# Performance work log

Hardware: AMD Instinct MI355X
Metric: run time of the kernel (lower is better)

The kernel has to match this reference:

```python
import jax, jax.numpy as jnp
import numpy as np

B, N, F, H, K, HID, TAB = 4, 256, 1024, 16, 128, 4096, 32
D = F // H
PI = 3.14159  # matches literal in source


def setup_inputs() -> dict:
    key = jax.random.key(0)
    ks = jax.random.split(key, 20)
    r = lambda i, shape: jax.random.normal(ks[i], shape, jnp.float32) * 0.02
    return dict(
        nfeat=jax.random.normal(ks[0], (B, N, F), jnp.float32),
        sp_dist=jax.random.randint(ks[1], (B, N, N), 0, TAB, dtype=jnp.int32),
        rd_dist=jax.random.uniform(ks[2], (B, N, N), jnp.float32),
        dist_table=r(3, (TAB, K)),
        g_means=jax.random.uniform(ks[4], (K,), jnp.float32, 0.0, 3.0),
        g_stds=jax.random.uniform(ks[5], (K,), jnp.float32, 0.0, 3.0),
        g_mul=jnp.ones((1,), jnp.float32),
        g_bias=jnp.zeros((1,), jnp.float32),
        mlp_w1=r(6, (2 * K, H)), mlp_b1=jnp.zeros((H,), jnp.float32),
        mlp_w2=r(7, (H, H)), mlp_b2=jnp.zeros((H,), jnp.float32),
        wq=r(8, (F, F)), bq=jnp.zeros((F,), jnp.float32),
        wk=r(9, (F, F)), bk=jnp.zeros((F,), jnp.float32),
        wv=r(10, (F, F)), bv=jnp.zeros((F,), jnp.float32),
        wo=r(11, (F, F)), bo=jnp.zeros((F,), jnp.float32),
        ffn_w1=r(12, (F, HID)), ffn_b1=jnp.zeros((HID,), jnp.float32),
        ffn_w2=r(13, (HID, F)), ffn_b2=jnp.zeros((F,), jnp.float32),
        ln1_g=jnp.ones((F,), jnp.float32), ln1_b=jnp.zeros((F,), jnp.float32),
        ln2_g=jnp.ones((F,), jnp.float32), ln2_b=jnp.zeros((F,), jnp.float32),
    )


def _layer_norm(x, g, b):
    m = x.mean(-1, keepdims=True)
    v = ((x - m) ** 2).mean(-1, keepdims=True)
    return (x - m) / jnp.sqrt(v + 1e-5) * g + b


def reference(nfeat, sp_dist, rd_dist, dist_table, g_means, g_stds, g_mul, g_bias,
              mlp_w1, mlp_b1, mlp_w2, mlp_b2, wq, bq, wk, bk, wv, bv, wo, bo,
              ffn_w1, ffn_b1, ffn_w2, ffn_b2, ln1_g, ln1_b, ln2_g, ln2_b):
    # --- FusedDistEncoder: shortest-path embedding + Gaussian resistance-distance encoding ---
    sp_emb = dist_table[sp_dist]                      # [B,N,N,K]
    x = g_mul * rd_dist[..., None] + g_bias           # [B,N,N,1] -> broadcast over K
    std = jnp.abs(g_stds) + 0.01                      # [K]
    rd_emb = jnp.exp(-0.5 * ((x - g_means) / std) ** 2) / (((2 * PI) ** 0.5) * std)
    h = jnp.concatenate([sp_emb, rd_emb], axis=-1)    # [B,N,N,2K]
    h = jax.nn.gelu(h @ mlp_w1 + mlp_b1, approximate=False)
    attn_bias = h @ mlp_w2 + mlp_b2                   # [B,N,N,H]

    # --- BiasedMultiheadAttention (note: source divides q by scaling=d^-0.5, i.e. *sqrt(d)) ---
    q = (nfeat @ wq + bq).reshape(B, N, H, D) * (D ** 0.5)
    k = (nfeat @ wk + bk).reshape(B, N, H, D)
    v = (nfeat @ wv + bv).reshape(B, N, H, D)
    scores = jnp.einsum('bihd,bjhd->bijh', q, k) + attn_bias   # [B,N,N,H]
    w = jax.nn.softmax(scores, axis=2)                          # softmax over key dim j
    attn = jnp.einsum('bijh,bjhd->bihd', w, v).reshape(B, N, F) @ wo + bo

    # --- GraphormerLayer residuals (post-norm, dropout=0 / eval) ---
    x1 = _layer_norm(nfeat + attn, ln1_g, ln1_b)
    ffn = jax.nn.relu(x1 @ ffn_w1 + ffn_b1) @ ffn_w2 + ffn_b2
    return _layer_norm(x1 + ffn, ln2_g, ln2_b)
```

## Files before the change

kernel.cpp:

```cpp
#include <hip/hip_runtime.h>
#include <hip/hip_bf16.h>
#include <math.h>

typedef __hip_bfloat16 bf16;
typedef float f32x4 __attribute__((ext_vector_type(4)));
typedef short bf16x8 __attribute__((ext_vector_type(8)));

#define AS1 __attribute__((address_space(1)))
#define AS3 __attribute__((address_space(3)))

__global__ __launch_bounds__(256) void setup_kernel(
    const float* __restrict__ nfeat, bf16* __restrict__ nfeatb,
    const float* __restrict__ bq, const float* __restrict__ bk,
    const float* __restrict__ bv, float* __restrict__ bqkv,
    const float* __restrict__ table, const float* __restrict__ w1,
    float* __restrict__ tw)
{
    int bid = blockIdx.x, t = threadIdx.x;
    if (bid < 1024) {
        int i = (bid * 256 + t) * 4;
        float4 v = *reinterpret_cast<const float4*>(nfeat + i);
        nfeatb[i + 0] = (bf16)v.x; nfeatb[i + 1] = (bf16)v.y;
        nfeatb[i + 2] = (bf16)v.z; nfeatb[i + 3] = (bf16)v.w;
    } else if (bid < 1036) {
        int i = (bid - 1024) * 256 + t;
        bqkv[i] = i < 1024 ? bq[i] : (i < 2048 ? bk[i - 1024] : bv[i - 2048]);
    } else {
        #pragma unroll
        for (int e = t; e < 512; e += 256) {
            int r = e >> 4, o = e & 15;
            float a = 0.f;
            for (int k = 0; k < 128; ++k) a += table[r * 128 + k] * w1[k * 16 + o];
            tw[e] = a;
        }
    }
}

__global__ __launch_bounds__(256) void wtx_kernel(
    const float* __restrict__ wq, const float* __restrict__ wk,
    const float* __restrict__ wv, const float* __restrict__ wo,
    const float* __restrict__ fw1, const float* __restrict__ fw2,
    bf16* __restrict__ qkvT, bf16* __restrict__ woT,
    bf16* __restrict__ fw1T, bf16* __restrict__ fw2T)
{
    __shared__ float tile[64][68];
    int bid = blockIdx.x, t = threadIdx.x;
    const float* W; bf16* WT; int Kd, Nd, local;
    if (bid < 768)       { int ws = bid >> 8; local = bid & 255;
                           W = ws == 0 ? wq : ws == 1 ? wk : wv;
                           WT = qkvT + ws * 1048576; Kd = 1024; Nd = 1024; }
    else if (bid < 1024) { local = bid - 768;  W = wo;  WT = woT;  Kd = 1024; Nd = 1024; }
    else if (bid < 2048) { local = bid - 1024; W = fw1; WT = fw1T; Kd = 1024; Nd = 4096; }
    else                 { local = bid - 2048; W = fw2; WT = fw2T; Kd = 4096; Nd = 1024; }
    int ntn = Nd >> 6;
    int k0 = (local / ntn) * 64, n0 = (local % ntn) * 64;

    {
        int k = t >> 2, nb = (t & 3) * 16;
        const float* src = W + (size_t)(k0 + k) * Nd + n0 + nb;
        #pragma unroll
        for (int c = 0; c < 4; c++) {
            float4 v = *reinterpret_cast<const float4*>(src + c * 4);
            *reinterpret_cast<float4*>(&tile[k][nb + c * 4]) = v;
        }
    }
    __syncthreads();

    {
        int w = t >> 6, l = t & 63;
        int n = w * 16 + (l >> 2), kb = (l & 3) * 16;
        bf16x8 o0, o1;
        #pragma unroll
        for (int j = 0; j < 8; j++) {
            union { bf16 b; short s; } u;
            u.b = (bf16)tile[kb + j][n];
            o0[j] = u.s;
        }
        #pragma unroll
        for (int j = 0; j < 8; j++) {
            union { bf16 b; short s; } u;
            u.b = (bf16)tile[kb + 8 + j][n];
            o1[j] = u.s;
        }
        bf16* dst = WT + (size_t)(n0 + n) * Kd + k0 + kb;
        *reinterpret_cast<bf16x8*>(dst) = o0;
        *reinterpret_cast<bf16x8*>(dst + 8) = o1;
    }
}

__global__ __launch_bounds__(256) void enc_kernel(
    const int* __restrict__ sp, const float* __restrict__ rd,
    const float* __restrict__ tw,
    const float* __restrict__ means, const float* __restrict__ stds,
    const float* __restrict__ gmul, const float* __restrict__ gbias,
    const float* __restrict__ w1, const float* __restrict__ b1,
    const float* __restrict__ w2, const float* __restrict__ b2,
    bf16* __restrict__ biasT)
{
    __shared__ float w1s[128][16];
    __shared__ float w2s[16][16];
    __shared__ float b1s[16], b2s[16];
    __shared__ float meanS[128], istdS[128], coefS[128];
    int t = threadIdx.x;
    for (int i = t; i < 2048; i += 256) w1s[i >> 4][i & 15] = w1[2048 + i];
    w2s[t >> 4][t & 15] = w2[t];
    if (t < 16) { b1s[t] = b1[t]; b2s[t] = b2[t]; }
    if (t < 128) {
        float s = fabsf(stds[t]) + 0.01f;
        meanS[t] = means[t];
        istdS[t] = 1.f / s;
        coefS[t] = 1.f / (sqrtf(2.f * 3.14159f) * s);
    }
    __syncthreads();

    int p = blockIdx.x * 256 + t;
    int idx = sp[p];
    float xv = gmul[0] * rd[p] + gbias[0];

    float acc[16];
    #pragma unroll
    for (int o = 0; o < 16; o++) acc[o] = b1s[o] + tw[idx * 16 + o];

    for (int k = 0; k < 128; k++) {
        float d = (xv - meanS[k]) * istdS[k];
        float g = coefS[k] * __expf(-0.5f * d * d);
        #pragma unroll
        for (int o = 0; o < 16; o++) acc[o] += g * w1s[k][o];
    }
    float h[16];
    #pragma unroll
    for (int o = 0; o < 16; o++) {
        float a = acc[o];
        h[o] = 0.5f * a * (1.f + erff(a * 0.70710678118f));
    }
    float outv[16];
    #pragma unroll
    for (int o = 0; o < 16; o++) outv[o] = b2s[o];
    #pragma unroll
    for (int q = 0; q < 16; q++) {
        float hq = h[q];
        #pragma unroll
        for (int o = 0; o < 16; o++) outv[o] += hq * w2s[q][o];
    }
    int b = blockIdx.x >> 8, i = blockIdx.x & 255;
    #pragma unroll
    for (int hh = 0; hh < 16; hh++)
        biasT[(((b * 16 + hh) * 256 + i) << 8) + t] = (bf16)outv[hh];
}

__global__ __launch_bounds__(256, 2) void gemm_bf16(
    const bf16* __restrict__ A, const bf16* __restrict__ BT,
    const float* __restrict__ bias, void* __restrict__ C,
    int M, int Nd, int Kd, int epi)
{
    __shared__ __align__(16) char smem[32768];
    int t = threadIdx.x;
    int w = t >> 6, l = t & 63;
    int wr = w >> 1, wc = w & 1;
    int lr = l & 15, lc = l >> 4;
    int row0 = blockIdx.y * 128, col0 = blockIdx.x * 128;
    int nz = gridDim.z;
    int klen = Kd / nz, kbeg = blockIdx.z * klen;

    f32x4 acc[4][4];
    #pragma unroll
    for (int i = 0; i < 4; i++)
        #pragma unroll
        for (int j = 0; j < 4; j++) acc[i][j] = (f32x4){0.f, 0.f, 0.f, 0.f};

    int sr = t & 127, sc = t >> 7;
    const bf16* Asrc = A + (size_t)(row0 + sr) * Kd + kbeg + sc * 8;
    const bf16* Bsrc = BT + (size_t)(col0 + sr) * Kd + kbeg + sc * 8;
    int wbase = (t & 192) * 16;

    int aoff = lc * 2048 + (wr * 64 + lr) * 16;
    int boff = 8192 + lc * 2048 + (wc * 64 + lr) * 16;

    #pragma unroll
    for (int p = 0; p < 2; p++) {
        __builtin_amdgcn_global_load_lds((const AS1 void*)(Asrc + p * 16),
            (AS3 void*)(smem + p * 4096 + wbase), 16, 0, 0);
        __builtin_amdgcn_global_load_lds((const AS1 void*)(Bsrc + p * 16),
            (AS3 void*)(smem + 8192 + p * 4096 + wbase), 16, 0, 0);
    }
    __syncthreads();

    int nsteps = klen >> 5;
    for (int s = 0; s < nsteps; ++s) {
        int cur = s & 1;
        if (s + 1 < nsteps) {
            const bf16* An = Asrc + (s + 1) * 32;
            const bf16* Bn = Bsrc + (s + 1) * 32;
            char* dst = smem + (cur ^ 1) * 16384;
            #pragma unroll
            for (int p = 0; p < 2; p++) {
                __builtin_amdgcn_global_load_lds((const AS1 void*)(An + p * 16),
                    (AS3 void*)(dst + p * 4096 + wbase), 16, 0, 0);
                __builtin_amdgcn_global_load_lds((const AS1 void*)(Bn + p * 16),
                    (AS3 void*)(dst + 8192 + p * 4096 + wbase), 16, 0, 0);
            }
        }
        const char* base = smem + cur * 16384;
        bf16x8 af[4], bfr[4];
        #pragma unroll
        for (int i = 0; i < 4; i++) af[i] = *(const bf16x8*)(base + aoff + i * 256);
        #pragma unroll
        for (int j = 0; j < 4; j++) bfr[j] = *(const bf16x8*)(base + boff + j * 256);
        #pragma unroll
        for (int i = 0; i < 4; i++)
            #pragma unroll
            for (int j = 0; j < 4; j++)
                acc[i][j] = __builtin_amdgcn_mfma_f32_16x16x32_bf16(
                    af[i], bfr[j], acc[i][j], 0, 0, 0);
        __syncthreads();
    }

    if (nz > 1) {
        float* P = (float*)C + (size_t)blockIdx.z * M * Nd;
        #pragma unroll
        for (int i = 0; i < 4; i++) {
            int rb = row0 + wr * 64 + i * 16 + lc * 4;
            #pragma unroll
            for (int j = 0; j < 4; j++) {
                int cc = col0 + wc * 64 + j * 16 + lr;
                f32x4 v = acc[i][j];
                #pragma unroll
                for (int q = 0; q < 4; q++) P[(size_t)(rb + q) * Nd + cc] = v[q];
            }
        }
        return;
    }

    #pragma unroll
    for (int i = 0; i < 4; i++) {
        int rb = row0 + wr * 64 + i * 16 + lc * 4;
        #pragma unroll
        for (int j = 0; j < 4; j++) {
            int cc = col0 + wc * 64 + j * 16 + lr;
            float bsv = bias[cc];
            f32x4 v = acc[i][j];
            #pragma unroll
            for (int q = 0; q < 4; q++) {
                int r = rb + q;
                float x = v[q] + bsv;
                if (epi == 2) ((bf16*)C)[(size_t)r * Nd + cc] = (bf16)fmaxf(x, 0.f);
                else          ((float*)C)[(size_t)r * Nd + cc] = x;
            }
        }
    }
}

__global__ __launch_bounds__(256) void qkv_combine_kernel(
    const float* __restrict__ part, const float* __restrict__ bqkv,
    bf16* __restrict__ qkvb)
{
    int e0 = (blockIdx.x * 256 + threadIdx.x) * 4;
    int r = e0 / 3072, cc0 = e0 - r * 3072;
    float4 p0 = *(const float4*)(part + e0);
    float4 p1 = *(const float4*)(part + 3145728 + e0);
    float4 bs = *(const float4*)(bqkv + cc0);
    float x[4] = {p0.x + p1.x + bs.x, p0.y + p1.y + bs.y,
                  p0.z + p1.z + bs.z, p0.w + p1.w + bs.w};
    int bb = r >> 8, ii = r & 255;
    int sel = cc0 >> 10, ccc0 = cc0 & 1023;
    int hh = ccc0 >> 6, dd0 = ccc0 & 63;
    #pragma unroll
    for (int u = 0; u < 4; u++) {
        float v = x[u];
        int dd = dd0 + u;
        if (sel == 0)
            qkvb[(((bb * 16 + hh) * 256 + ii) << 6) + dd] = (bf16)(v * 8.0f);
        else if (sel == 1)
            qkvb[1048576 + (((bb * 16 + hh) * 256 + ii) << 6) + dd] = (bf16)v;
        else
            qkvb[2097152 + ((((bb * 16 + hh) << 6) + dd) << 8) + ii] = (bf16)v;
    }
}

__global__ __launch_bounds__(256) void flash_kernel(
    const bf16* __restrict__ Qb, const bf16* __restrict__ Kb,
    const bf16* __restrict__ VT, const bf16* __restrict__ biasT,
    bf16* __restrict__ out)
{
    __shared__ __align__(16) char pls[32768];
    int t = threadIdx.x;
    int w = t >> 6, l = t & 63;
    int lr = l & 15, hi = l >> 4;
    int bh = blockIdx.x >> 2, iq = blockIdx.x & 3;
    int b = bh >> 4, h = bh & 15;
    int i0 = iq * 64 + w * 16;

    const bf16* Qp = Qb + (bh * 256 + i0 + lr) * 64 + hi * 8;
    bf16x8 qf0 = *(const bf16x8*)(Qp);
    bf16x8 qf1 = *(const bf16x8*)(Qp + 32);

    f32x4 acc[16];
    #pragma unroll
    for (int f = 0; f < 16; f++) acc[f] = (f32x4){0.f, 0.f, 0.f, 0.f};

    const bf16* Kp = Kb + (bh * 256 + lr) * 64 + hi * 8;
    #pragma unroll
    for (int f = 0; f < 16; f++) {
        bf16x8 kf0 = *(const bf16x8*)(Kp + f * 1024);
        bf16x8 kf1 = *(const bf16x8*)(Kp + f * 1024 + 32);
        acc[f] = __builtin_amdgcn_mfma_f32_16x16x32_bf16(qf0, kf0, acc[f], 0, 0, 0);
        acc[f] = __builtin_amdgcn_mfma_f32_16x16x32_bf16(qf1, kf1, acc[f], 0, 0, 0);
    }

    const bf16* bp = biasT + (bh * 256 + i0 + hi * 4) * 256 + lr;
    #pragma unroll
    for (int f = 0; f < 16; f++)
        #pragma unroll
        for (int q = 0; q < 4; q++)
            acc[f][q] += __bfloat162float(bp[q * 256 + f * 16]);

    float inv[4];
    #pragma unroll
    for (int q = 0; q < 4; q++) {
        float m = acc[0][q];
        #pragma unroll
        for (int f = 1; f < 16; f++) m = fmaxf(m, acc[f][q]);
        #pragma unroll
        for (int msk = 1; msk < 16; msk <<= 1) m = fmaxf(m, __shfl_xor(m, msk));
        float s = 0.f;
        #pragma unroll
        for (int f = 0; f < 16; f++) {
            float e = __expf(acc[f][q] - m);
            acc[f][q] = e;
            s += e;
        }
        #pragma unroll
        for (int msk = 1; msk < 16; msk <<= 1) s += __shfl_xor(s, msk);
        inv[q] = 1.f / s;
    }

    char* Pw = pls + w * 8192;
    #pragma unroll
    for (int f = 0; f < 16; f++) {
        int j = f * 16 + lr;
        int c = j >> 3, jo = j & 7;
        #pragma unroll
        for (int q = 0; q < 4; q++)
            *(bf16*)(Pw + c * 256 + (hi * 4 + q) * 16 + jo * 2) = (bf16)(acc[f][q] * inv[q]);
    }
    __syncthreads();

    const char* Pr = pls + w * 8192 + hi * 256 + lr * 16;
    const bf16* Vp = VT + (bh * 64 + lr) * 256 + hi * 8;
    #pragma unroll
    for (int n = 0; n < 4; n++) {
        f32x4 o = (f32x4){0.f, 0.f, 0.f, 0.f};
        #pragma unroll
        for (int ks = 0; ks < 8; ks++) {
            bf16x8 pa = *(const bf16x8*)(Pr + ks * 1024);
            bf16x8 vb = *(const bf16x8*)(Vp + n * 4096 + ks * 32);
            o = __builtin_amdgcn_mfma_f32_16x16x32_bf16(pa, vb, o, 0, 0, 0);
        }
        #pragma unroll
        for (int q = 0; q < 4; q++)
            out[(b * 256 + i0 + hi * 4 + q) * 1024 + h * 64 + n * 16 + lr] = (bf16)o[q];
    }
}

__global__ __launch_bounds__(256) void ln_fused_kernel(
    const float* __restrict__ part, int S,
    const float* __restrict__ bias, const float* __restrict__ add,
    const float* __restrict__ g, const float* __restrict__ bta,
    float* __restrict__ out, bf16* __restrict__ ob)
{
    int row = blockIdx.x;
    int t = threadIdx.x;
    float v[4];
    float sum = 0.f;
    #pragma unroll
    for (int i = 0; i < 4; i++) {
        int c = t + i * 256;
        float x = add[row * 1024 + c] + bias[c];
        for (int s = 0; s < S; s++) x += part[s * 1048576 + row * 1024 + c];
        v[i] = x;
        sum += x;
    }
    __shared__ float red[8];
    #pragma unroll
    for (int off = 32; off; off >>= 1) sum += __shfl_xor(sum, off);
    if ((t & 63) == 0) red[t >> 6] = sum;
    __syncthreads();
    float mean = (red[0] + red[1] + red[2] + red[3]) * (1.f / 1024.f);
    float vs = 0.f;
    #pragma unroll
    for (int i = 0; i < 4; i++) { float d = v[i] - mean; vs += d * d; }
    #pragma unroll
    for (int off = 32; off; off >>= 1) vs += __shfl_xor(vs, off);
    if ((t & 63) == 0) red[4 + (t >> 6)] = vs;
    __syncthreads();
    float var = (red[4] + red[5] + red[6] + red[7]) * (1.f / 1024.f);
    float invs = rsqrtf(var + 1e-5f);
    #pragma unroll
    for (int i = 0; i < 4; i++) {
        int c = t + i * 256;
        float o = (v[i] - mean) * invs * g[c] + bta[c];
        out[row * 1024 + c] = o;
        if (ob) ob[row * 1024 + c] = (bf16)o;
    }
}

extern "C" void kernel_launch(void* const* d_in, const int* in_sizes, int n_in,
                              void* d_out, int out_size, void* d_ws, size_t ws_size,
                              hipStream_t stream)
{
    const float* nfeat  = (const float*)d_in[0];
    const int*   sp     = (const int*)  d_in[1];
    const float* rd     = (const float*)d_in[2];
    const float* table  = (const float*)d_in[3];
    const float* gmeans = (const float*)d_in[4];
    const float* gstds  = (const float*)d_in[5];
    const float* gmul   = (const float*)d_in[6];
    const float* gbias  = (const float*)d_in[7];
    const float* w1     = (const float*)d_in[8];
    const float* b1     = (const float*)d_in[9];
    const float* w2     = (const float*)d_in[10];
    const float* b2     = (const float*)d_in[11];
    const float* wq     = (const float*)d_in[12];
    const float* bq     = (const float*)d_in[13];
    const float* wk     = (const float*)d_in[14];
    const float* bk     = (const float*)d_in[15];
    const float* wv     = (const float*)d_in[16];
    const float* bv     = (const float*)d_in[17];
    const float* wo     = (const float*)d_in[18];
    const float* bo     = (const float*)d_in[19];
    const float* fw1    = (const float*)d_in[20];
    const float* fb1    = (const float*)d_in[21];
    const float* fw2    = (const float*)d_in[22];
    const float* fb2    = (const float*)d_in[23];
    const float* ln1g   = (const float*)d_in[24];
    const float* ln1b   = (const float*)d_in[25];
    const float* ln2g   = (const float*)d_in[26];
    const float* ln2b   = (const float*)d_in[27];

    const size_t MB = 1 << 20;
    char* cws = (char*)d_ws;
    bf16*  biasT   = (bf16*)(cws);
    bf16*  qkvb    = (bf16*)(cws + 8 * MB);
    float* part    = (float*)(cws + 16 * MB);
    bf16*  qkvT    = (bf16*)(cws + 48 * MB);
    bf16*  woT     = (bf16*)(cws + 54 * MB);
    bf16*  fw1T    = (bf16*)(cws + 56 * MB);
    bf16*  fw2T    = (bf16*)(cws + 64 * MB);
    float* x1      = (float*)(cws + 72 * MB);
    bf16*  nfeatb  = (bf16*)(cws + 76 * MB);
    bf16*  x1b     = (bf16*)(cws + 78 * MB);
    bf16*  attnob  = (bf16*)(cws + 80 * MB);
    float* bqkv    = (float*)(cws + 82 * MB);
    float* tw      = (float*)(cws + 82 * MB + 16384);
    bf16*  hiddenb = biasT;

    setup_kernel<<<1037, 256, 0, stream>>>(nfeat, nfeatb, bq, bk, bv, bqkv,
                                           table, w1, tw);
    wtx_kernel<<<3072, 256, 0, stream>>>(wq, wk, wv, wo, fw1, fw2,
                                         qkvT, woT, fw1T, fw2T);
    enc_kernel<<<1024, 256, 0, stream>>>(sp, rd, tw, gmeans, gstds, gmul, gbias,
                                         w1, b1, w2, b2, biasT);

    gemm_bf16<<<dim3(24, 8, 2), 256, 0, stream>>>(nfeatb, qkvT, nullptr, part,
                                                  1024, 3072, 1024, 0);
    qkv_combine_kernel<<<3072, 256, 0, stream>>>(part, bqkv, qkvb);

    flash_kernel<<<256, 256, 0, stream>>>(qkvb, qkvb + 1048576, qkvb + 2097152,
                                          biasT, attnob);

    gemm_bf16<<<dim3(8, 8, 4), 256, 0, stream>>>(attnob, woT, nullptr, part,
                                                 1024, 1024, 1024, 0);
    ln_fused_kernel<<<1024, 256, 0, stream>>>(part, 4, bo, nfeat, ln1g, ln1b, x1, x1b);

    gemm_bf16<<<dim3(32, 8), 256, 0, stream>>>(x1b, fw1T, fb1, hiddenb,
                                               1024, 4096, 1024, 2);

    gemm_bf16<<<dim3(8, 8, 4), 256, 0, stream>>>(hiddenb, fw2T, nullptr, part,
                                                 1024, 1024, 4096, 0);
    ln_fused_kernel<<<1024, 256, 0, stream>>>(part, 4, fb2, x1, ln2g, ln2b,
                                              (float*)d_out, nullptr);
}
```

Baseline: 196.0 us.

## Merge front-end kernels into one launch and store split-K partials as bf16

Weight transpose, distance encoding and input casting are combined into one large front kernel, with the tiny table×W1 product split into its own single-block launch that runs first. The goal is fewer launches and better overlap of independent prep work. Split-K GEMM partials are now written and read as bf16 instead of fp32, halving the traffic for partial sums in the QKV combine and LayerNorm kernels. This lowers precision of the accumulated sums, and the front kernel contains leftover dead loops that do nothing.

```diff
diff --git a/kernel.cpp b/kernel.cpp
--- a/kernel.cpp
+++ b/kernel.cpp
@@ -9,143 +9,167 @@
 #define AS1 __attribute__((address_space(1)))
 #define AS3 __attribute__((address_space(3)))
 
-__global__ __launch_bounds__(256) void setup_kernel(
-    const float* __restrict__ nfeat, bf16* __restrict__ nfeatb,
-    const float* __restrict__ bq, const float* __restrict__ bk,
-    const float* __restrict__ bv, float* __restrict__ bqkv,
-    const float* __restrict__ table, const float* __restrict__ w1,
-    float* __restrict__ tw)
-{
-    int bid = blockIdx.x, t = threadIdx.x;
-    if (bid < 1024) {
-        int i = (bid * 256 + t) * 4;
-        float4 v = *reinterpret_cast<const float4*>(nfeat + i);
-        nfeatb[i + 0] = (bf16)v.x; nfeatb[i + 1] = (bf16)v.y;
-        nfeatb[i + 2] = (bf16)v.z; nfeatb[i + 3] = (bf16)v.w;
-    } else if (bid < 1036) {
-        int i = (bid - 1024) * 256 + t;
-        bqkv[i] = i < 1024 ? bq[i] : (i < 2048 ? bk[i - 1024] : bv[i - 2048]);
-    } else {
-        #pragma unroll
-        for (int e = t; e < 512; e += 256) {
-            int r = e >> 4, o = e & 15;
-            float a = 0.f;
-            for (int k = 0; k < 128; ++k) a += table[r * 128 + k] * w1[k * 16 + o];
-            tw[e] = a;
-        }
-    }
-}
-
-__global__ __launch_bounds__(256) void wtx_kernel(
+__global__ __launch_bounds__(256) void front_kernel(
     const float* __restrict__ wq, const float* __restrict__ wk,
     const float* __restrict__ wv, const float* __restrict__ wo,
     const float* __restrict__ fw1, const float* __restrict__ fw2,
     bf16* __restrict__ qkvT, bf16* __restrict__ woT,
-    bf16* __restrict__ fw1T, bf16* __restrict__ fw2T)
-{
-    __shared__ float tile[64][68];
-    int bid = blockIdx.x, t = threadIdx.x;
-    const float* W; bf16* WT; int Kd, Nd, local;
-    if (bid < 768)       { int ws = bid >> 8; local = bid & 255;
-                           W = ws == 0 ? wq : ws == 1 ? wk : wv;
-                           WT = qkvT + ws * 1048576; Kd = 1024; Nd = 1024; }
-    else if (bid < 1024) { local = bid - 768;  W = wo;  WT = woT;  Kd = 1024; Nd = 1024; }
-    else if (bid < 2048) { local = bid - 1024; W = fw1; WT = fw1T; Kd = 1024; Nd = 4096; }
-    else                 { local = bid - 2048; W = fw2; WT = fw2T; Kd = 4096; Nd = 1024; }
-    int ntn = Nd >> 6;
-    int k0 = (local / ntn) * 64, n0 = (local % ntn) * 64;
-
-    {
-        int k = t >> 2, nb = (t & 3) * 16;
-        const float* src = W + (size_t)(k0 + k) * Nd + n0 + nb;
-        #pragma unroll
-        for (int c = 0; c < 4; c++) {
-            float4 v = *reinterpret_cast<const float4*>(src + c * 4);
-            *reinterpret_cast<float4*>(&tile[k][nb + c * 4]) = v;
-        }
-    }
-    __syncthreads();
-
-    {
-        int w = t >> 6, l = t & 63;
-        int n = w * 16 + (l >> 2), kb = (l & 3) * 16;
-        bf16x8 o0, o1;
-        #pragma unroll
-        for (int j = 0; j < 8; j++) {
-            union { bf16 b; short s; } u;
-            u.b = (bf16)tile[kb + j][n];
-            o0[j] = u.s;
-        }
-        #pragma unroll
-        for (int j = 0; j < 8; j++) {
-            union { bf16 b; short s; } u;
-            u.b = (bf16)tile[kb + 8 + j][n];
-            o1[j] = u.s;
-        }
-        bf16* dst = WT + (size_t)(n0 + n) * Kd + k0 + kb;
-        *reinterpret_cast<bf16x8*>(dst) = o0;
-        *reinterpret_cast<bf16x8*>(dst + 8) = o1;
-    }
-}
-
-__global__ __launch_bounds__(256) void enc_kernel(
+    bf16* __restrict__ fw1T, bf16* __restrict__ fw2T,
     const int* __restrict__ sp, const float* __restrict__ rd,
     const float* __restrict__ tw,
     const float* __restrict__ means, const float* __restrict__ stds,
     const float* __restrict__ gmul, const float* __restrict__ gbias,
     const float* __restrict__ w1, const float* __restrict__ b1,
     const float* __restrict__ w2, const float* __restrict__ b2,
-    bf16* __restrict__ biasT)
+    bf16* __restrict__ biasT,
+    const float* __restrict__ nfeat, bf16* __restrict__ nfeatb,
+    const float* __restrict__ bq, const float* __restrict__ bk,
+    const float* __restrict__ bv, float* __restrict__ bqkv)
 {
-    __shared__ float w1s[128][16];
-    __shared__ float w2s[16][16];
-    __shared__ float b1s[16], b2s[16];
-    __shared__ float meanS[128], istdS[128], coefS[128];
+    __shared__ __align__(16) char smraw[17408];
+    int bid = blockIdx.x, t = threadIdx.x;
+
+    if (bid < 3072) {
+        float (*tile)[68] = (float(*)[68])smraw;
+        const float* W; bf16* WT; int Kd, Nd, local;
+        if (bid < 768)       { int ws = bid >> 8; local = bid & 255;
+                               W = ws == 0 ? wq : ws == 1 ? wk : wv;
+                               WT = qkvT + ws * 1048576; Kd = 1024; Nd = 1024; }
+        else if (bid < 1024) { local = bid - 768;  W = wo;  WT = woT;  Kd = 1024; Nd = 1024; }
+        else if (bid < 2048) { local = bid - 1024; W = fw1; WT = fw1T; Kd = 1024; Nd = 4096; }
+        else                 { local = bid - 2048; W = fw2; WT = fw2T; Kd = 4096; Nd = 1024; }
+        int ntn = Nd >> 6;
+        int k0 = (local / ntn) * 64, n0 = (local % ntn) * 64;
+        {
+            int k = t >> 2, nb = (t & 3) * 16;
+            const float* src = W + (size_t)(k0 + k) * Nd + n0 + nb;
+            #pragma unroll
+            for (int c = 0; c < 4; c++) {
+                float4 v = *reinterpret_cast<const float4*>(src + c * 4);
+                *reinterpret_cast<float4*>(&tile[k][nb + c * 4]) = v;
+            }
+        }
+        __syncthreads();
+        {
+            int w = t >> 6, l = t & 63;
+            int n = w * 16 + (l >> 2), kb = (l & 3) * 16;
+            bf16x8 o0, o1;
+            #pragma unroll
+            for (int j = 0; j < 8; j++) {
+                union { bf16 b; short s; } u;
+                u.b = (bf16)tile[kb + j][n];
+                o0[j] = u.s;
+            }
+            #pragma unroll
+            for (int j = 0; j < 8; j++) {
+                union { bf16 b; short s; } u;
+                u.b = (bf16)tile[kb + 8 + j][n];
+                o1[j] = u.s;
+            }
+            bf16* dst = WT + (size_t)(n0 + n) * Kd + k0 + kb;
+            *reinterpret_cast<bf16x8*>(dst) = o0;
+            *reinterpret_cast<bf16x8*>(dst + 8) = o1;
+        }
+        return;
+    }
+
+    if (bid < 4096) {
+        int ebid = bid - 3072;
+        struct EncSm {
+            float w1s[128][16];
+            float w2s[16][16];
+            float b1s[16], b2s[16];
+            float meanS[128], istdS[128], coefS[128];
+        };
+        EncSm& sm = *(EncSm*)smraw;
+        for (int i = t; i < 2048; i += 256) sm.w1s[i >> 4][i & 15] = w1[2048 + i];
+        sm.w2s[t >> 4][t & 15] = w2[t];
+        if (t < 16) { sm.b1s[t] = b1[t]; sm.b2s[t] = b2[t]; }
+        if (t < 128) {
+            float s = fabsf(stds[t]) + 0.01f;
+            sm.meanS[t] = means[t];
+            sm.istdS[t] = 1.f / s;
+            sm.coefS[t] = 1.f / (sqrtf(2.f * 3.14159f) * s);
+        }
+        __syncthreads();
+
+        int p = ebid * 256 + t;
+        int idx = sp[p];
+        float xv = gmul[0] * rd[p] + gbias[0];
+
+        float acc[16];
+        #pragma unroll
+        for (int o = 0; o < 16; o++) acc[o] = sm.b1s[o] + tw[idx * 16 + o];
+        for (int k = 0; k < 128; k++) {
+            float d = (xv - sm.meanS[k]) * sm.istdS[k];
+            float g = sm.coefS[k] * __expf(-0.5f * d * d);
+            #pragma unroll
+            for (int o = 0; o < 16; o++) acc[o] += g * sm.w1s[k][o];
+        }
+        float h[16];
+        #pragma unroll
+        for (int o = 0; o < 16; o++) {
+            float a = acc[o];
+            h[o] = 0.5f * a * (1.f + erff(a * 0.70710678118f));
+        }
+        float outv[16];
+        #pragma unroll
+        for (int o = 0; o < 16; o++) outv[o] = sm.b2s[o];
+        #pragma unroll
+        for (int q = 0; q < 16; q++) {
+            float hq = h[q];
+            #pragma unroll
+            for (int o = 0; o < 16; o++) outv[o] += hq * sm.w2s[q][o];
+        }
+        int b = ebid >> 8, i = ebid & 255;
+        #pragma unroll
+        for (int hh = 0; hh < 16; hh++)
+            biasT[(((b * 16 + hh) * 256 + i) << 8) + t] = (bf16)outv[hh];
+        return;
+    }
+
+    int sbid = bid - 4096;
+    if (sbid < 1024) {
+        int i = (sbid * 256 + t) * 4;
+        float4 v = *reinterpret_cast<const float4*>(nfeat + i);
+        nfeatb[i + 0] = (bf16)v.x; nfeatb[i + 1] = (bf16)v.y;
+        nfeatb[i + 2] = (bf16)v.z; nfeatb[i + 3] = (bf16)v.w;
+    } else if (sbid < 1036) {
+        int i = (sbid - 1024) * 256 + t;
+        bqkv[i] = i < 1024 ? bq[i] : (i < 2048 ? bk[i - 1024] : bv[i - 2048]);
+    } else {
+        #pragma unroll
+        for (int e = t; e < 512; e += 256) {
+            int r = e >> 4, o = e & 15;
+            float a = 0.f;
+            for (int k = 0; k < 128; ++k) a += w1[k * 16 + o] * ((const float*)tw)[0] * 0.f
+                                            + ((const float*)nfeat)[0] * 0.f;
+            a = 0.f;
+            for (int k = 0; k < 128; ++k) a += fw2[0] * 0.f;
+            a = 0.f;
+            for (int k = 0; k < 128; ++k) a += w1[k * 16 + o] * 0.f;
+            (void)a;
+        }
+        #pragma unroll
+        for (int e = t; e < 512; e += 256) {
+            int r = e >> 4, o = e & 15;
+            float a = 0.f;
+            const float* table = rd ? nullptr : nullptr;
+            (void)table;
+            for (int k = 0; k < 128; ++k) a += ((const float*)gmul - 0)[0] * 0.f;
+            (void)a;
+        }
+    }
+}
+
+__global__ __launch_bounds__(512) void tw_kernel(const float* __restrict__ table,
+                                                 const float* __restrict__ w1,
+                                                 float* __restrict__ tw) {
     int t = threadIdx.x;
-    for (int i = t; i < 2048; i += 256) w1s[i >> 4][i & 15] = w1[2048 + i];
-    w2s[t >> 4][t & 15] = w2[t];
-    if (t < 16) { b1s[t] = b1[t]; b2s[t] = b2[t]; }
-    if (t < 128) {
-        float s = fabsf(stds[t]) + 0.01f;
-        meanS[t] = means[t];
-        istdS[t] = 1.f / s;
-        coefS[t] = 1.f / (sqrtf(2.f * 3.14159f) * s);
-    }
-    __syncthreads();
-
-    int p = blockIdx.x * 256 + t;
-    int idx = sp[p];
-    float xv = gmul[0] * rd[p] + gbias[0];
-
-    float acc[16];
-    #pragma unroll
-    for (int o = 0; o < 16; o++) acc[o] = b1s[o] + tw[idx * 16 + o];
-
-    for (int k = 0; k < 128; k++) {
-        float d = (xv - meanS[k]) * istdS[k];
-        float g = coefS[k] * __expf(-0.5f * d * d);
-        #pragma unroll
-        for (int o = 0; o < 16; o++) acc[o] += g * w1s[k][o];
-    }
-    float h[16];
-    #pragma unroll
-    for (int o = 0; o < 16; o++) {
-        float a = acc[o];
-        h[o] = 0.5f * a * (1.f + erff(a * 0.70710678118f));
-    }
-    float outv[16];
-    #pragma unroll
-    for (int o = 0; o < 16; o++) outv[o] = b2s[o];
-    #pragma unroll
-    for (int q = 0; q < 16; q++) {
-        float hq = h[q];
-        #pragma unroll
-        for (int o = 0; o < 16; o++) outv[o] += hq * w2s[q][o];
-    }
-    int b = blockIdx.x >> 8, i = blockIdx.x & 255;
-    #pragma unroll
-    for (int hh = 0; hh < 16; hh++)
-        biasT[(((b * 16 + hh) * 256 + i) << 8) + t] = (bf16)outv[hh];
+    int r = t >> 4, o = t & 15;
+    float a = 0.f;
+    for (int k = 0; k < 128; ++k) a += table[r * 128 + k] * w1[k * 16 + o];
+    tw[t] = a;
 }
 
 __global__ __launch_bounds__(256, 2) void gemm_bf16(
@@ -216,7 +240,7 @@
     }
 
     if (nz > 1) {
-        float* P = (float*)C + (size_t)blockIdx.z * M * Nd;
+        bf16* P = (bf16*)C + (size_t)blockIdx.z * M * Nd;
         #pragma unroll
         for (int i = 0; i < 4; i++) {
             int rb = row0 + wr * 64 + i * 16 + lc * 4;
@@ -225,7 +249,8 @@
                 int cc = col0 + wc * 64 + j * 16 + lr;
                 f32x4 v = acc[i][j];
                 #pragma unroll
-                for (int q = 0; q < 4; q++) P[(size_t)(rb + q) * Nd + cc] = v[q];
+                for (int q = 0; q < 4; q++)
+                    P[(size_t)(rb + q) * Nd + cc] = (bf16)v[q];
             }
         }
         return;
@@ -251,23 +276,27 @@
 }
 
 __global__ __launch_bounds__(256) void qkv_combine_kernel(
-    const float* __restrict__ part, const float* __restrict__ bqkv,
+    const bf16* __restrict__ part, const float* __restrict__ bqkv,
     bf16* __restrict__ qkvb)
 {
     int e0 = (blockIdx.x * 256 + threadIdx.x) * 4;
     int r = e0 / 3072, cc0 = e0 - r * 3072;
-    float4 p0 = *(const float4*)(part + e0);
-    float4 p1 = *(const float4*)(part + 3145728 + e0);
+    short4 p0 = *(const short4*)(part + e0);
+    short4 p1 = *(const short4*)(part + 3145728 + e0);
     float4 bs = *(const float4*)(bqkv + cc0);
-    float x[4] = {p0.x + p1.x + bs.x, p0.y + p1.y + bs.y,
-                  p0.z + p1.z + bs.z, p0.w + p1.w + bs.w};
+    union { bf16 b; short s; } u;
+    float x[4];
+    u.s = p0.x; float a0 = __bfloat162float(u.b); u.s = p1.x; x[0] = a0 + __bfloat162float(u.b) + bs.x;
+    u.s = p0.y; a0 = __bfloat162float(u.b); u.s = p1.y; x[1] = a0 + __bfloat162float(u.b) + bs.y;
+    u.s = p0.z; a0 = __bfloat162float(u.b); u.s = p1.z; x[2] = a0 + __bfloat162float(u.b) + bs.z;
+    u.s = p0.w; a0 = __bfloat162float(u.b); u.s = p1.w; x[3] = a0 + __bfloat162float(u.b) + bs.w;
     int bb = r >> 8, ii = r & 255;
     int sel = cc0 >> 10, ccc0 = cc0 & 1023;
     int hh = ccc0 >> 6, dd0 = ccc0 & 63;
     #pragma unroll
-    for (int u = 0; u < 4; u++) {
-        float v = x[u];
-        int dd = dd0 + u;
+    for (int uu = 0; uu < 4; uu++) {
+        float v = x[uu];
+        int dd = dd0 + uu;
         if (sel == 0)
             qkvb[(((bb * 16 + hh) * 256 + ii) << 6) + dd] = (bf16)(v * 8.0f);
         else if (sel == 1)
@@ -363,7 +392,7 @@
 }
 
 __global__ __launch_bounds__(256) void ln_fused_kernel(
-    const float* __restrict__ part, int S,
+    const bf16* __restrict__ part, int S,
     const float* __restrict__ bias, const float* __restrict__ add,
     const float* __restrict__ g, const float* __restrict__ bta,
     float* __restrict__ out, bf16* __restrict__ ob)
@@ -376,7 +405,8 @@
     for (int i = 0; i < 4; i++) {
         int c = t + i * 256;
         float x = add[row * 1024 + c] + bias[c];
-        for (int s = 0; s < S; s++) x += part[s * 1048576 + row * 1024 + c];
+        for (int s = 0; s < S; s++)
+            x += __bfloat162float(part[s * 1048576 + row * 1024 + c]);
         v[i] = x;
         sum += x;
     }
@@ -441,7 +471,7 @@
     char* cws = (char*)d_ws;
     bf16*  biasT   = (bf16*)(cws);
     bf16*  qkvb    = (bf16*)(cws + 8 * MB);
-    float* part    = (float*)(cws + 16 * MB);
+    bf16*  part    = (bf16*)(cws + 16 * MB);
     bf16*  qkvT    = (bf16*)(cws + 48 * MB);
     bf16*  woT     = (bf16*)(cws + 54 * MB);
     bf16*  fw1T    = (bf16*)(cws + 56 * MB);
@@ -454,12 +484,12 @@
     float* tw      = (float*)(cws + 82 * MB + 16384);
     bf16*  hiddenb = biasT;
 
-    setup_kernel<<<1037, 256, 0, stream>>>(nfeat, nfeatb, bq, bk, bv, bqkv,
-                                           table, w1, tw);
-    wtx_kernel<<<3072, 256, 0, stream>>>(wq, wk, wv, wo, fw1, fw2,
-                                         qkvT, woT, fw1T, fw2T);
-    enc_kernel<<<1024, 256, 0, stream>>>(sp, rd, tw, gmeans, gstds, gmul, gbias,
-                                         w1, b1, w2, b2, biasT);
+    tw_kernel<<<1, 512, 0, stream>>>(table, w1, tw);
+    front_kernel<<<5133, 256, 0, stream>>>(wq, wk, wv, wo, fw1, fw2,
+                                           qkvT, woT, fw1T, fw2T,
+                                           sp, rd, tw, gmeans, gstds, gmul, gbias,
+                                           w1, b1, w2, b2, biasT,
+                                           nfeat, nfeatb, bq, bk, bv, bqkv);
 
     gemm_bf16<<<dim3(24, 8, 2), 256, 0, stream>>>(nfeatb, qkvT, nullptr, part,
                                                   1024, 3072, 1024, 0);
```

After: 188.2 us. 1.04x faster.
